# Kernel optimization log

Measured on AMD Instinct MI355X. Metric: run time of the kernel, lower is better.

## Reference

```python
import jax, jax.numpy as jnp
import numpy as np

N = 100000   # nodes
E = 3200000  # edges (avg degree 32)
D = 2        # spatial dim (2D collective motion)
C = 1.0      # spring constant c
R_C = 1.0    # rest length r_c
P = 2        # potential exponent p
GAMMA = 0.1  # damping gamma
EPS = 1e-12  # torch F.normalize eps


def setup_inputs() -> dict:
    key = jax.random.key(0)
    k1, k2, k3, k4 = jax.random.split(key, 4)
    x = jax.random.normal(k1, (N, D), dtype=jnp.float32) * 10.0  # positions
    v = jax.random.normal(k2, (N, D), dtype=jnp.float32)          # velocities
    src = jax.random.randint(k3, (E,), 0, N)                      # edge sources
    dst = jax.random.randint(k4, (E,), 0, N)                      # edge destinations
    return {"x": x, "v": v, "src": src, "dst": dst}


def reference(x, v, src, dst):
    # calc_message: dr = dst_pos - src_pos (non-periodic euclid distance)
    dr = x[dst] - x[src]                                   # [E, D]
    abs_dr = jnp.linalg.norm(dr, axis=-1, keepdims=True)   # [E, 1]
    unit_dr = dr / jnp.maximum(abs_dr, EPS)                # F.normalize
    force = -C * P * (abs_dr - R_C) ** (P - 1)             # spring force magnitude
    m = force * unit_dr                                    # [E, D] message
    # update_all: fn.sum of messages at dst nodes -> acceleration
    a = jax.ops.segment_sum(m, dst, num_segments=N)        # [N, D]
    # damping term
    return a - GAMMA * v
```

## Files before the change

kernel.cpp:

```cpp
#include <hip/hip_runtime.h>

#define GAMMA 0.1f
#define EPS_F 1e-12f

#define S_NODES 200
#define PMAX 512
#define BK 256
#define BK_THREADS 1024

__global__ __launch_bounds__(BK_THREADS)
void count_kernel(const int4* __restrict__ dst4, const int* __restrict__ dst,
                  int* __restrict__ cnts, int e, int chunk) {
    __shared__ int hist[PMAX];
    int tid = threadIdx.x, b = blockIdx.x;
    for (int i = tid; i < PMAX; i += BK_THREADS) hist[i] = 0;
    __syncthreads();
    int e4 = e >> 2;
    long gs = (long)b * chunk;
    long ge = gs + chunk; if (ge > e4) ge = e4;
    for (long i = gs + tid; i < ge; i += BK_THREADS) {
        int4 d4 = dst4[i];
        atomicAdd(&hist[d4.x / S_NODES], 1);
        atomicAdd(&hist[d4.y / S_NODES], 1);
        atomicAdd(&hist[d4.z / S_NODES], 1);
        atomicAdd(&hist[d4.w / S_NODES], 1);
    }
    if (b == BK - 1) {
        for (int i = e4 * 4 + tid; i < e; i += BK_THREADS)
            atomicAdd(&hist[dst[i] / S_NODES], 1);
    }
    __syncthreads();
    for (int k = tid; k < PMAX; k += BK_THREADS)
        cnts[(long)k * BK + b] = hist[k];
}

__global__ __launch_bounds__(1024)
void colscan_kernel(int* __restrict__ cnts, int* __restrict__ totals) {
    int wid = (blockIdx.x * blockDim.x + threadIdx.x) >> 6;
    int lane = threadIdx.x & 63;
    if (wid >= PMAX) return;
    int4* col = (int4*)(cnts + (long)wid * BK);
    int4 vv = col[lane];
    int lt = vv.x + vv.y + vv.z + vv.w;
    int inc = lt;
    #pragma unroll
    for (int off = 1; off < 64; off <<= 1) {
        int t = __shfl_up(inc, off);
        if (lane >= off) inc += t;
    }
    int ex = inc - lt;
    int4 bb;
    bb.x = ex;
    bb.y = ex + vv.x;
    bb.z = ex + vv.x + vv.y;
    bb.w = ex + vv.x + vv.y + vv.z;
    col[lane] = bb;
    if (lane == 63) totals[wid] = inc;
}

__global__ __launch_bounds__(PMAX)
void prefix_kernel(const int* __restrict__ totals, int* __restrict__ starts) {
    __shared__ int sc[PMAX];
    int k = threadIdx.x;
    int t = totals[k];
    sc[k] = t;
    __syncthreads();
    for (int off = 1; off < PMAX; off <<= 1) {
        int vv = (k >= off) ? sc[k - off] : 0;
        __syncthreads();
        sc[k] += vv;
        __syncthreads();
    }
    starts[k] = sc[k] - t;
    if (k == PMAX - 1) starts[PMAX] = sc[k];
}

__device__ __forceinline__ void scatter_one(int s, int d, int* loff,
                                            int* __restrict__ buckets) {
    int p = d / S_NODES;
    int r = atomicAdd(&loff[p], 1);
    buckets[r] = (s << 8) | (d - p * S_NODES);
}

__global__ __launch_bounds__(BK_THREADS)
void scatter_kernel(const int4* __restrict__ src4, const int4* __restrict__ dst4,
                    const int* __restrict__ src, const int* __restrict__ dst,
                    const int* __restrict__ cnts, const int* __restrict__ starts,
                    int* __restrict__ buckets, int e, int chunk) {
    __shared__ int loff[PMAX];
    int tid = threadIdx.x, b = blockIdx.x;
    for (int i = tid; i < PMAX; i += BK_THREADS)
        loff[i] = cnts[(long)i * BK + b] + starts[i];
    __syncthreads();
    int e4 = e >> 2;
    long gs = (long)b * chunk;
    long ge = gs + chunk; if (ge > e4) ge = e4;
    for (long i = gs + tid; i < ge; i += BK_THREADS) {
        int4 s4 = src4[i];
        int4 d4 = dst4[i];
        scatter_one(s4.x, d4.x, loff, buckets);
        scatter_one(s4.y, d4.y, loff, buckets);
        scatter_one(s4.z, d4.z, loff, buckets);
        scatter_one(s4.w, d4.w, loff, buckets);
    }
    if (b == BK - 1) {
        for (int i = e4 * 4 + tid; i < e; i += BK_THREADS)
            scatter_one(src[i], dst[i], loff, buckets);
    }
}

__global__ __launch_bounds__(1024)
void scan_kernel(const float2* __restrict__ x, const float2* __restrict__ v,
                 const int* __restrict__ buckets, const int* __restrict__ starts,
                 float2* __restrict__ out, int n) {
    __shared__ float2 acc[S_NODES];
    int k = blockIdx.x, tid = threadIdx.x;
    int lo = k * S_NODES;
    for (int i = tid; i < S_NODES; i += 1024) acc[i] = make_float2(0.f, 0.f);
    __syncthreads();
    int s0 = starts[k], s1 = starts[k + 1];
    for (int i = s0 + tid; i < s1; i += 1024) {
        int w = buckets[i];
        int s = w >> 8;
        int dl = w & 255;
        float2 xs = x[s];
        float2 xd = x[lo + dl];
        float dx = xd.x - xs.x;
        float dy = xd.y - xs.y;
        float r = sqrtf(dx * dx + dy * dy);
        float sc = -2.0f * (r - 1.0f) / fmaxf(r, EPS_F);
        atomicAdd(&acc[dl].x, sc * dx);
        atomicAdd(&acc[dl].y, sc * dy);
    }
    __syncthreads();
    for (int i = tid; i < S_NODES; i += 1024) {
        int g = lo + i;
        if (g < n) {
            float2 vi = v[g];
            out[g] = make_float2(acc[i].x - GAMMA * vi.x,
                                 acc[i].y - GAMMA * vi.y);
        }
    }
}

__global__ void init_out_kernel(const float2* __restrict__ v,
                                float2* __restrict__ out, int n) {
    int i = blockIdx.x * blockDim.x + threadIdx.x;
    if (i < n) {
        float2 vi = v[i];
        out[i] = make_float2(-GAMMA * vi.x, -GAMMA * vi.y);
    }
}

__device__ __forceinline__ void do_edge_atomic(const float2* __restrict__ x,
                                               int s, int d,
                                               float* __restrict__ out) {
    float2 xs = x[s];
    float2 xd = x[d];
    float dx = xd.x - xs.x;
    float dy = xd.y - xs.y;
    float r = sqrtf(dx * dx + dy * dy);
    float sc = -2.0f * (r - 1.0f) / fmaxf(r, EPS_F);
    atomicAdd(&out[2 * d], sc * dx);
    atomicAdd(&out[2 * d + 1], sc * dy);
}

__global__ void edge_kernel_atomic(const float2* __restrict__ x,
                                   const int4* __restrict__ src4,
                                   const int4* __restrict__ dst4,
                                   const int* __restrict__ src,
                                   const int* __restrict__ dst,
                                   float* __restrict__ out,
                                   int e4, int e_total) {
    int i = blockIdx.x * blockDim.x + threadIdx.x;
    if (i < e4) {
        int4 s = src4[i];
        int4 d = dst4[i];
        do_edge_atomic(x, s.x, d.x, out);
        do_edge_atomic(x, s.y, d.y, out);
        do_edge_atomic(x, s.z, d.z, out);
        do_edge_atomic(x, s.w, d.w, out);
    }
    if (i == 0) {
        for (int ee = e4 * 4; ee < e_total; ++ee)
            do_edge_atomic(x, src[ee], dst[ee], out);
    }
}

extern "C" void kernel_launch(void* const* d_in, const int* in_sizes, int n_in,
                              void* d_out, int out_size, void* d_ws, size_t ws_size,
                              hipStream_t stream) {
    const float2* x = (const float2*)d_in[0];
    const float2* v = (const float2*)d_in[1];
    const int* src  = (const int*)d_in[2];
    const int* dst  = (const int*)d_in[3];

    int n = in_sizes[0] / 2;
    int e = in_sizes[2];

    float2* out = (float2*)d_out;

    int P = (n + S_NODES - 1) / S_NODES;

    size_t off_totals = (size_t)PMAX * BK * sizeof(int);
    size_t off_starts = off_totals + PMAX * sizeof(int);
    size_t off_buckets = (off_starts + (PMAX + 1) * sizeof(int) + 255) & ~(size_t)255;
    size_t need = off_buckets + (size_t)e * sizeof(int);

    if (P <= PMAX && n < (1 << 24) && ws_size >= need) {
        int* cnts = (int*)d_ws;
        int* totals = (int*)((char*)d_ws + off_totals);
        int* starts = (int*)((char*)d_ws + off_starts);
        int* buckets = (int*)((char*)d_ws + off_buckets);

        int e4 = e >> 2;
        int chunk = (e4 + BK - 1) / BK;

        count_kernel<<<BK, BK_THREADS, 0, stream>>>(
            (const int4*)dst, dst, cnts, e, chunk);
        colscan_kernel<<<(PMAX * 64) / 1024, 1024, 0, stream>>>(cnts, totals);
        prefix_kernel<<<1, PMAX, 0, stream>>>(totals, starts);
        scatter_kernel<<<BK, BK_THREADS, 0, stream>>>(
            (const int4*)src, (const int4*)dst, src, dst,
            cnts, starts, buckets, e, chunk);
        scan_kernel<<<P, 1024, 0, stream>>>(
            x, v, buckets, starts, out, n);
    } else {
        int threads = 256;
        init_out_kernel<<<(n + threads - 1) / threads, threads, 0, stream>>>(
            v, out, n);
        int e4 = e / 4;
        int blocks = (e4 + threads - 1) / threads;
        if (blocks < 1) blocks = 1;
        edge_kernel_atomic<<<blocks, threads, 0, stream>>>(
            x, (const int4*)src, (const int4*)dst, src, dst, (float*)out, e4, e);
    }
}
```

Measured before the change: 138.9 us.

## Use coarser dst partitions, split each across blocks, add partial-sum reduce

Dst partitions grow from 200 to 1600 nodes, which cuts the partition count to 63. Each partition is split across 8 blocks of 256 threads that accumulate into private shared-memory partial sums, and a new reduce kernel sums the 8 partials and applies damping. The column scan and prefix kernels are merged into a single launch, and the bucket encoding uses 11 bits for the local index. This is meant to reduce launch count and per-edge histogram contention, at the cost of an extra partials buffer, an extra kernel, and more scatter contention on fewer bins.

New measurement: 132.8 us. -4.4%, faster.

```diff
diff --git a/kernel.cpp b/kernel.cpp
--- a/kernel.cpp
+++ b/kernel.cpp
@@ -3,17 +3,19 @@
 #define GAMMA 0.1f
 #define EPS_F 1e-12f
 
-#define S_NODES 200
-#define PMAX 512
+#define S_NODES 1600
+#define PMAX 64
 #define BK 256
 #define BK_THREADS 1024
+#define SCAN_B 8
+#define SCAN_THREADS 256
 
 __global__ __launch_bounds__(BK_THREADS)
 void count_kernel(const int4* __restrict__ dst4, const int* __restrict__ dst,
                   int* __restrict__ cnts, int e, int chunk) {
     __shared__ int hist[PMAX];
     int tid = threadIdx.x, b = blockIdx.x;
-    for (int i = tid; i < PMAX; i += BK_THREADS) hist[i] = 0;
+    if (tid < PMAX) hist[tid] = 0;
     __syncthreads();
     int e4 = e >> 2;
     long gs = (long)b * chunk;
@@ -30,56 +32,52 @@
             atomicAdd(&hist[dst[i] / S_NODES], 1);
     }
     __syncthreads();
-    for (int k = tid; k < PMAX; k += BK_THREADS)
-        cnts[(long)k * BK + b] = hist[k];
+    if (tid < PMAX) cnts[(long)tid * BK + b] = hist[tid];
 }
 
 __global__ __launch_bounds__(1024)
-void colscan_kernel(int* __restrict__ cnts, int* __restrict__ totals) {
-    int wid = (blockIdx.x * blockDim.x + threadIdx.x) >> 6;
-    int lane = threadIdx.x & 63;
-    if (wid >= PMAX) return;
-    int4* col = (int4*)(cnts + (long)wid * BK);
-    int4 vv = col[lane];
-    int lt = vv.x + vv.y + vv.z + vv.w;
-    int inc = lt;
-    #pragma unroll
-    for (int off = 1; off < 64; off <<= 1) {
-        int t = __shfl_up(inc, off);
-        if (lane >= off) inc += t;
-    }
-    int ex = inc - lt;
-    int4 bb;
-    bb.x = ex;
-    bb.y = ex + vv.x;
-    bb.z = ex + vv.x + vv.y;
-    bb.w = ex + vv.x + vv.y + vv.z;
-    col[lane] = bb;
-    if (lane == 63) totals[wid] = inc;
-}
-
-__global__ __launch_bounds__(PMAX)
-void prefix_kernel(const int* __restrict__ totals, int* __restrict__ starts) {
+void scanoff_kernel(int* __restrict__ cnts, int* __restrict__ starts) {
     __shared__ int sc[PMAX];
-    int k = threadIdx.x;
-    int t = totals[k];
-    sc[k] = t;
-    __syncthreads();
+    int tid = threadIdx.x;
+    int wave = tid >> 6, lane = tid & 63;
+    for (int col = wave; col < PMAX; col += 16) {
+        int4* colp = (int4*)(cnts + (long)col * BK);
+        int4 vv = colp[lane];
+        int lt = vv.x + vv.y + vv.z + vv.w;
+        int inc = lt;
+        #pragma unroll
+        for (int off = 1; off < 64; off <<= 1) {
+            int t = __shfl_up(inc, off);
+            if (lane >= off) inc += t;
+        }
+        int ex = inc - lt;
+        int4 bb;
+        bb.x = ex;
+        bb.y = ex + vv.x;
+        bb.z = ex + vv.x + vv.y;
+        bb.w = ex + vv.x + vv.y + vv.z;
+        colp[lane] = bb;
+        if (lane == 63) sc[col] = inc;
+    }
+    __syncthreads();
+    int tot = (tid < PMAX) ? sc[tid] : 0;
     for (int off = 1; off < PMAX; off <<= 1) {
-        int vv = (k >= off) ? sc[k - off] : 0;
+        int vv = (tid < PMAX && tid >= off) ? sc[tid - off] : 0;
         __syncthreads();
-        sc[k] += vv;
+        if (tid < PMAX) sc[tid] += vv;
         __syncthreads();
     }
-    starts[k] = sc[k] - t;
-    if (k == PMAX - 1) starts[PMAX] = sc[k];
+    if (tid < PMAX) {
+        starts[tid] = sc[tid] - tot;
+        if (tid == PMAX - 1) starts[PMAX] = sc[tid];
+    }
 }
 
 __device__ __forceinline__ void scatter_one(int s, int d, int* loff,
                                             int* __restrict__ buckets) {
     int p = d / S_NODES;
     int r = atomicAdd(&loff[p], 1);
-    buckets[r] = (s << 8) | (d - p * S_NODES);
+    buckets[r] = (s << 11) | (d - p * S_NODES);
 }
 
 __global__ __launch_bounds__(BK_THREADS)
@@ -89,8 +87,8 @@
                     int* __restrict__ buckets, int e, int chunk) {
     __shared__ int loff[PMAX];
     int tid = threadIdx.x, b = blockIdx.x;
-    for (int i = tid; i < PMAX; i += BK_THREADS)
-        loff[i] = cnts[(long)i * BK + b] + starts[i];
+    if (tid < PMAX)
+        loff[tid] = cnts[(long)tid * BK + b] + starts[tid];
     __syncthreads();
     int e4 = e >> 2;
     long gs = (long)b * chunk;
@@ -109,20 +107,27 @@
     }
 }
 
-__global__ __launch_bounds__(1024)
-void scan_kernel(const float2* __restrict__ x, const float2* __restrict__ v,
+__global__ __launch_bounds__(SCAN_THREADS)
+void scan_kernel(const float2* __restrict__ x,
                  const int* __restrict__ buckets, const int* __restrict__ starts,
-                 float2* __restrict__ out, int n) {
+                 float2* __restrict__ partials) {
     __shared__ float2 acc[S_NODES];
-    int k = blockIdx.x, tid = threadIdx.x;
-    int lo = k * S_NODES;
-    for (int i = tid; i < S_NODES; i += 1024) acc[i] = make_float2(0.f, 0.f);
-    __syncthreads();
-    int s0 = starts[k], s1 = starts[k + 1];
-    for (int i = s0 + tid; i < s1; i += 1024) {
+    int p = blockIdx.x / SCAN_B;
+    int b = blockIdx.x - p * SCAN_B;
+    int lo = p * S_NODES;
+    int tid = threadIdx.x;
+    for (int i = tid; i < S_NODES; i += SCAN_THREADS)
+        acc[i] = make_float2(0.f, 0.f);
+    __syncthreads();
+    int s0 = starts[p], s1 = starts[p + 1];
+    int len = s1 - s0;
+    int ch = (len + SCAN_B - 1) / SCAN_B;
+    int a0 = s0 + b * ch;
+    int a1 = a0 + ch; if (a1 > s1) a1 = s1;
+    for (int i = a0 + tid; i < a1; i += SCAN_THREADS) {
         int w = buckets[i];
-        int s = w >> 8;
-        int dl = w & 255;
+        int s = ((unsigned)w) >> 11;
+        int dl = w & 2047;
         float2 xs = x[s];
         float2 xd = x[lo + dl];
         float dx = xd.x - xs.x;
@@ -133,14 +138,32 @@
         atomicAdd(&acc[dl].y, sc * dy);
     }
     __syncthreads();
-    for (int i = tid; i < S_NODES; i += 1024) {
-        int g = lo + i;
-        if (g < n) {
-            float2 vi = v[g];
-            out[g] = make_float2(acc[i].x - GAMMA * vi.x,
-                                 acc[i].y - GAMMA * vi.y);
-        }
-    }
+    float2* wsb = partials + (size_t)blockIdx.x * S_NODES;
+    for (int i = tid; i < S_NODES; i += SCAN_THREADS)
+        wsb[i] = acc[i];
+}
+
+__global__ __launch_bounds__(256)
+void reduce_kernel(const float2* __restrict__ partials,
+                   const float2* __restrict__ v,
+                   float2* __restrict__ out, int n) {
+    int i = blockIdx.x * blockDim.x + threadIdx.x;
+    if (i >= n) return;
+    int p = i / S_NODES;
+    int loc = i - p * S_NODES;
+    const float2* base = partials + ((size_t)(p * SCAN_B) * S_NODES + loc);
+    float2 t0 = base[0 * S_NODES];
+    float2 t1 = base[1 * S_NODES];
+    float2 t2 = base[2 * S_NODES];
+    float2 t3 = base[3 * S_NODES];
+    float2 t4 = base[4 * S_NODES];
+    float2 t5 = base[5 * S_NODES];
+    float2 t6 = base[6 * S_NODES];
+    float2 t7 = base[7 * S_NODES];
+    float sx = ((t0.x + t1.x) + (t2.x + t3.x)) + ((t4.x + t5.x) + (t6.x + t7.x));
+    float sy = ((t0.y + t1.y) + (t2.y + t3.y)) + ((t4.y + t5.y) + (t6.y + t7.y));
+    float2 vi = v[i];
+    out[i] = make_float2(sx - GAMMA * vi.x, sy - GAMMA * vi.y);
 }
 
 __global__ void init_out_kernel(const float2* __restrict__ v,
@@ -202,29 +225,30 @@
 
     int P = (n + S_NODES - 1) / S_NODES;
 
-    size_t off_totals = (size_t)PMAX * BK * sizeof(int);
-    size_t off_starts = off_totals + PMAX * sizeof(int);
+    size_t off_starts = (size_t)PMAX * BK * sizeof(int);
     size_t off_buckets = (off_starts + (PMAX + 1) * sizeof(int) + 255) & ~(size_t)255;
-    size_t need = off_buckets + (size_t)e * sizeof(int);
-
-    if (P <= PMAX && n < (1 << 24) && ws_size >= need) {
+    size_t off_part = (off_buckets + (size_t)e * sizeof(int) + 255) & ~(size_t)255;
+    size_t need = off_part + (size_t)P * SCAN_B * S_NODES * sizeof(float2);
+
+    if (P <= PMAX && n <= (1 << 20) && ws_size >= need) {
         int* cnts = (int*)d_ws;
-        int* totals = (int*)((char*)d_ws + off_totals);
         int* starts = (int*)((char*)d_ws + off_starts);
         int* buckets = (int*)((char*)d_ws + off_buckets);
+        float2* partials = (float2*)((char*)d_ws + off_part);
 
         int e4 = e >> 2;
         int chunk = (e4 + BK - 1) / BK;
 
         count_kernel<<<BK, BK_THREADS, 0, stream>>>(
             (const int4*)dst, dst, cnts, e, chunk);
-        colscan_kernel<<<(PMAX * 64) / 1024, 1024, 0, stream>>>(cnts, totals);
-        prefix_kernel<<<1, PMAX, 0, stream>>>(totals, starts);
+        scanoff_kernel<<<1, 1024, 0, stream>>>(cnts, starts);
         scatter_kernel<<<BK, BK_THREADS, 0, stream>>>(
             (const int4*)src, (const int4*)dst, src, dst,
             cnts, starts, buckets, e, chunk);
-        scan_kernel<<<P, 1024, 0, stream>>>(
-            x, v, buckets, starts, out, n);
+        scan_kernel<<<P * SCAN_B, SCAN_THREADS, 0, stream>>>(
+            x, buckets, starts, partials);
+        reduce_kernel<<<(n + 255) / 256, 256, 0, stream>>>(
+            partials, v, out, n);
     } else {
         int threads = 256;
         init_out_kernel<<<(n + threads - 1) / threads, threads, 0, stream>>>(
```
